# Optimization experiments

Measured on AMD Instinct MI355X. Metric: run time of the kernel, lower is better.

## Reference

```python
import jax, jax.numpy as jnp
import numpy as np

NEG_SLOPE = 0.2
EPS = 1e-16


def gatv2_conv(x, src, dst, n_nodes, Wl, Wr, att, bias):
    """GATv2Conv, heads=1, add_self_loops handled by caller via src/dst.
    x: [N, Fin]; src/dst: [E] (message j->i means src=j, dst=i).
    Wl, Wr: [Fin, Fout]; att: [Fout]; bias: [Fout].
    """
    xl = x @ Wl  # [N, Fout] (source transform)
    xr = x @ Wr  # [N, Fout] (target transform)
    # per-edge attention logit: a^T LeakyReLU(xl[j] + xr[i])
    h = xl[src] + xr[dst]                      # [E, Fout]
    e = jax.nn.leaky_relu(h, NEG_SLOPE) @ att  # [E]
    # segment softmax over incoming edges of each dst node
    m = jax.ops.segment_max(e, dst, num_segments=n_nodes)   # [N]
    ex = jnp.exp(e - m[dst])                                 # [E]
    denom = jax.ops.segment_sum(ex, dst, num_segments=n_nodes)  # [N]
    alpha = ex / (denom[dst] + EPS)                          # [E]
    # scatter-aggregate weighted source messages
    out = jax.ops.segment_sum(alpha[:, None] * xl[src], dst, num_segments=n_nodes)
    return out + bias


def glorot(key, shape):
    lim = np.sqrt(6.0 / (shape[0] + shape[1]))
    return jax.random.uniform(key, shape, jnp.float32, -lim, lim)


def setup_inputs() -> dict:
    key = jax.random.key(0)
    ks = jax.random.split(key, 9)
    N, E, Fin, H, Fout = 50000, 800000, 128, 64, 2
    x = jax.random.normal(ks[0], (N, Fin), jnp.float32)
    edge_index = jax.random.randint(ks[1], (2, E), 0, N, jnp.int64)
    return {
        "x": x,
        "edge_index": edge_index,
        "Wl1": glorot(ks[2], (Fin, H)),
        "Wr1": glorot(ks[3], (Fin, H)),
        "att1": glorot(ks[4], (H, 1))[:, 0],
        "b1": jnp.zeros((H,), jnp.float32),
        "Wl2": glorot(ks[5], (H, Fout)),
        "Wr2": glorot(ks[6], (H, Fout)),
        "att2": glorot(ks[7], (Fout, 1))[:, 0],
        "b2": jnp.zeros((Fout,), jnp.float32),
    }


def reference(x, edge_index, Wl1, Wr1, att1, b1, Wl2, Wr2, att2, b2):
    n_nodes = x.shape[0]
    # PyG GATv2Conv adds self-loops by default
    loops = jnp.arange(n_nodes, dtype=edge_index.dtype)
    src = jnp.concatenate([edge_index[0], loops])
    dst = jnp.concatenate([edge_index[1], loops])
    # eval mode: dropout is identity; the initial relu/dropout result is dead code
    h = gatv2_conv(x, src, dst, n_nodes, Wl1, Wr1, att1, b1)
    out = gatv2_conv(h, src, dst, n_nodes, Wl2, Wr2, att2, b2)
    return out
```

## Files before the change

kernel.cpp:

```cpp
#include <hip/hip_runtime.h>
#include <math.h>

#define FIN 128
#define H 64
#define FOUT 2
#define NEG_SLOPE 0.2f
#define EPS 1e-16f

#define BM 64
#define BK 32
#define SCAN_CHUNK 2048

__global__ void k_zero_int(int* __restrict__ a, int n){
  int i = blockIdx.x*blockDim.x + threadIdx.x;
  if(i < n) a[i] = 0;
}

__global__ __launch_bounds__(256) void k_gemm1(
    const float* __restrict__ x, const float* __restrict__ Wl,
    const float* __restrict__ Wr, float* __restrict__ xl,
    float* __restrict__ xr, int N){
  __shared__ float xsT[BK][BM+4];
  __shared__ float ws[BK][128];
  int tid = threadIdx.x;
  int rowbase = blockIdx.x*BM;
  int tc = tid & 15, tr = tid >> 4;
  int r0 = tr*4, c0 = tc*4;
  float acc[4][8];
  #pragma unroll
  for(int i=0;i<4;i++)
    #pragma unroll
    for(int j=0;j<8;j++) acc[i][j]=0.f;

  int lrow = tid >> 2;
  int lk8  = (tid & 3) * 8;
  int wkk  = tid >> 3;
  int wfq  = tid & 7;

  for(int k0=0; k0<FIN; k0+=BK){
    __syncthreads();
    {
      int grow = rowbase + lrow;
      float4 v0 = make_float4(0,0,0,0), v1 = make_float4(0,0,0,0);
      if(grow < N){
        v0 = *(const float4*)(x + (size_t)grow*FIN + k0 + lk8);
        v1 = *(const float4*)(x + (size_t)grow*FIN + k0 + lk8 + 4);
      }
      xsT[lk8+0][lrow]=v0.x; xsT[lk8+1][lrow]=v0.y; xsT[lk8+2][lrow]=v0.z; xsT[lk8+3][lrow]=v0.w;
      xsT[lk8+4][lrow]=v1.x; xsT[lk8+5][lrow]=v1.y; xsT[lk8+6][lrow]=v1.z; xsT[lk8+7][lrow]=v1.w;
    }
    #pragma unroll
    for(int i=0;i<4;i++){
      int c4 = (wfq + i*8)*4;
      const float* srcp = (c4 < 64) ? (Wl + (size_t)(k0+wkk)*H + c4)
                                    : (Wr + (size_t)(k0+wkk)*H + (c4-64));
      *(float4*)(&ws[wkk][c4]) = *(const float4*)srcp;
    }
    __syncthreads();
    #pragma unroll
    for(int kk=0; kk<BK; kk++){
      float4 av = *(float4*)(&xsT[kk][r0]);
      float4 b0 = *(float4*)(&ws[kk][c0]);
      float4 b1 = *(float4*)(&ws[kk][64+c0]);
      float a[4] = {av.x,av.y,av.z,av.w};
      float b[8] = {b0.x,b0.y,b0.z,b0.w,b1.x,b1.y,b1.z,b1.w};
      #pragma unroll
      for(int i=0;i<4;i++)
        #pragma unroll
        for(int j=0;j<8;j++)
          acc[i][j] += a[i]*b[j];
    }
  }
  #pragma unroll
  for(int i=0;i<4;i++){
    int row = rowbase + r0 + i;
    if(row < N){
      *(float4*)(xl + (size_t)row*H + c0) = make_float4(acc[i][0],acc[i][1],acc[i][2],acc[i][3]);
      *(float4*)(xr + (size_t)row*H + c0) = make_float4(acc[i][4],acc[i][5],acc[i][6],acc[i][7]);
    }
  }
}

__global__ void k_degree(const int* __restrict__ ei, int E, int Etot,
                         int* __restrict__ deg, int* __restrict__ rank){
  int i0 = (blockIdx.x*blockDim.x + threadIdx.x)*4;
  if(i0 >= Etot) return;
  if(i0 + 4 <= E && (E & 3) == 0){
    int4 d4 = *(const int4*)(ei + E + i0);
    int r0 = atomicAdd(&deg[d4.x],1);
    int r1 = atomicAdd(&deg[d4.y],1);
    int r2 = atomicAdd(&deg[d4.z],1);
    int r3 = atomicAdd(&deg[d4.w],1);
    *(int4*)(rank + i0) = make_int4(r0,r1,r2,r3);
  } else if(i0 >= E && i0 + 4 <= Etot){
    int v = i0 - E;
    int r0 = atomicAdd(&deg[v+0],1);
    int r1 = atomicAdd(&deg[v+1],1);
    int r2 = atomicAdd(&deg[v+2],1);
    int r3 = atomicAdd(&deg[v+3],1);
    *(int4*)(rank + i0) = make_int4(r0,r1,r2,r3);
  } else {
    #pragma unroll
    for(int q=0;q<4;q++){
      int i = i0+q; if(i>=Etot) break;
      int dst = (i<E) ? ei[E+i] : (i-E);
      rank[i] = atomicAdd(&deg[dst],1);
    }
  }
}

__global__ __launch_bounds__(256) void k_scan_a(const int* __restrict__ deg, int n,
                                                int* __restrict__ rowptr,
                                                int* __restrict__ blocksum){
  __shared__ int wsum[4];
  int tid = threadIdx.x, lane = tid & 63, wid = tid >> 6;
  int idx = blockIdx.x*SCAN_CHUNK + tid*8;
  int v[8];
  if(idx + 8 <= n){
    int4 a = *(const int4*)(deg + idx);
    int4 b = *(const int4*)(deg + idx + 4);
    v[0]=a.x;v[1]=a.y;v[2]=a.z;v[3]=a.w;v[4]=b.x;v[5]=b.y;v[6]=b.z;v[7]=b.w;
  } else {
    #pragma unroll
    for(int i=0;i<8;i++) v[i] = (idx+i<n)? deg[idx+i] : 0;
  }
  int pre[8]; int st=0;
  #pragma unroll
  for(int i=0;i<8;i++){ pre[i]=st; st+=v[i]; }
  int incl = st;
  #pragma unroll
  for(int o=1;o<64;o<<=1){ int u=__shfl_up(incl,o); if(lane>=o) incl+=u; }
  if(lane==63) wsum[wid]=incl;
  __syncthreads();
  if(tid==0){ int accu=0; for(int i=0;i<4;i++){ int t=wsum[i]; wsum[i]=accu; accu+=t; } }
  __syncthreads();
  int toff = wsum[wid] + incl - st;
  if(idx + 8 <= n){
    int4 o0 = make_int4(toff+pre[0],toff+pre[1],toff+pre[2],toff+pre[3]);
    int4 o1 = make_int4(toff+pre[4],toff+pre[5],toff+pre[6],toff+pre[7]);
    *(int4*)(rowptr+idx)=o0; *(int4*)(rowptr+idx+4)=o1;
  } else {
    #pragma unroll
    for(int i=0;i<8;i++) if(idx+i<n) rowptr[idx+i]=toff+pre[i];
  }
  if(tid==255) blocksum[blockIdx.x] = toff + st;
}

__global__ void k_scan_b(int* __restrict__ blocksum, int nb, int* __restrict__ rowptr, int n){
  int lane = threadIdx.x & 63;
  int v = (lane<nb)? blocksum[lane] : 0;
  int incl = v;
  #pragma unroll
  for(int o=1;o<64;o<<=1){ int u=__shfl_up(incl,o); if(lane>=o) incl+=u; }
  if(lane<nb) blocksum[lane] = incl - v;
  if(lane==63) rowptr[n] = incl;
}

__global__ void k_scan_c(int* __restrict__ rowptr, const int* __restrict__ blocksum, int n){
  int i = blockIdx.x*blockDim.x + threadIdx.x;
  if(i<n) rowptr[i] += blocksum[i >> 11];
}

__global__ void k_fill(const int* __restrict__ ei, int E, int Etot,
                       const int* __restrict__ rowptr,
                       const int* __restrict__ rank, int* __restrict__ csr_src){
  int i0 = (blockIdx.x*blockDim.x + threadIdx.x)*4;
  if(i0 >= Etot) return;
  if(i0 + 4 <= E && (E & 3) == 0){
    int4 s4 = *(const int4*)(ei + i0);
    int4 d4 = *(const int4*)(ei + E + i0);
    int4 r4 = *(const int4*)(rank + i0);
    csr_src[rowptr[d4.x] + r4.x] = s4.x;
    csr_src[rowptr[d4.y] + r4.y] = s4.y;
    csr_src[rowptr[d4.z] + r4.z] = s4.z;
    csr_src[rowptr[d4.w] + r4.w] = s4.w;
  } else if(i0 >= E && i0 + 4 <= Etot){
    int4 r4 = *(const int4*)(rank + i0);
    int v = i0 - E;
    csr_src[rowptr[v+0] + r4.x] = v+0;
    csr_src[rowptr[v+1] + r4.y] = v+1;
    csr_src[rowptr[v+2] + r4.z] = v+2;
    csr_src[rowptr[v+3] + r4.w] = v+3;
  } else {
    #pragma unroll
    for(int q=0;q<4;q++){
      int i = i0+q; if(i>=Etot) break;
      int src, dst;
      if(i<E){ src = ei[i]; dst = ei[E+i]; } else { src = i-E; dst = i-E; }
      csr_src[rowptr[dst] + rank[i]] = src;
    }
  }
}

__global__ void k_node1f(const int* __restrict__ rowptr, const int* __restrict__ csr_src,
                         const float* __restrict__ xl, const float* __restrict__ xr,
                         const float* __restrict__ att, const float* __restrict__ b1,
                         const float* __restrict__ Wl2, const float* __restrict__ Wr2,
                         float* __restrict__ xl2, float* __restrict__ xr2, int N){
  int node = blockIdx.x*16 + (threadIdx.x>>4);
  int gl = threadIdx.x & 15;
  if(node >= N) return;
  int f4 = gl*4;
  float4 attv = *(const float4*)(att + f4);
  float4 xrv  = *(const float4*)(xr + (size_t)node*H + f4);
  int s = rowptr[node], t = rowptr[node+1];
  float d = 0.f;
  float ax=0.f, ay=0.f, az=0.f, aw=0.f;

  for(int k=s; k<t; k+=8){
    int tl = t - 1;
    int ks[8]; float4 xv[8]; float msk[8];
    #pragma unroll
    for(int j=0;j<8;j++){
      int kj = k + j;
      ks[j] = (kj < t) ? kj : tl;
      msk[j] = (kj < t) ? 1.f : 0.f;
    }
    int ss[8];
    #pragma unroll
    for(int j=0;j<8;j++) ss[j] = csr_src[ks[j]];
    #pragma unroll
    for(int j=0;j<8;j++) xv[j] = *(const float4*)(xl + (size_t)ss[j]*H + f4);
    #pragma unroll
    for(int j=0;j<8;j++){
      float h0 = xv[j].x + xrv.x, h1 = xv[j].y + xrv.y;
      float h2 = xv[j].z + xrv.z, h3 = xv[j].w + xrv.w;
      float l0 = (h0>0.f)? h0 : NEG_SLOPE*h0;
      float l1 = (h1>0.f)? h1 : NEG_SLOPE*h1;
      float l2 = (h2>0.f)? h2 : NEG_SLOPE*h2;
      float l3 = (h3>0.f)? h3 : NEG_SLOPE*h3;
      float e = l0*attv.x + l1*attv.y + l2*attv.z + l3*attv.w;
      #pragma unroll
      for(int o=1;o<16;o<<=1) e += __shfl_xor(e,o);
      float w = msk[j] * __expf(e);
      d  += w;
      ax += w*xv[j].x; ay += w*xv[j].y; az += w*xv[j].z; aw += w*xv[j].w;
    }
  }

  float inv = 1.f/(d + EPS);
  float4 bv = *(const float4*)(b1 + f4);
  float h0 = ax*inv + bv.x, h1 = ay*inv + bv.y;
  float h2 = az*inv + bv.z, h3 = aw*inv + bv.w;
  float p0 = h0*Wl2[(f4+0)*FOUT+0] + h1*Wl2[(f4+1)*FOUT+0] + h2*Wl2[(f4+2)*FOUT+0] + h3*Wl2[(f4+3)*FOUT+0];
  float p1 = h0*Wl2[(f4+0)*FOUT+1] + h1*Wl2[(f4+1)*FOUT+1] + h2*Wl2[(f4+2)*FOUT+1] + h3*Wl2[(f4+3)*FOUT+1];
  float p2 = h0*Wr2[(f4+0)*FOUT+0] + h1*Wr2[(f4+1)*FOUT+0] + h2*Wr2[(f4+2)*FOUT+0] + h3*Wr2[(f4+3)*FOUT+0];
  float p3 = h0*Wr2[(f4+0)*FOUT+1] + h1*Wr2[(f4+1)*FOUT+1] + h2*Wr2[(f4+2)*FOUT+1] + h3*Wr2[(f4+3)*FOUT+1];
  #pragma unroll
  for(int o=1;o<16;o<<=1){
    p0 += __shfl_xor(p0,o); p1 += __shfl_xor(p1,o);
    p2 += __shfl_xor(p2,o); p3 += __shfl_xor(p3,o);
  }
  if(gl==0){
    *(float2*)(xl2 + node*2) = make_float2(p0,p1);
    *(float2*)(xr2 + node*2) = make_float2(p2,p3);
  }
}

__global__ void k_node2(const int* __restrict__ rowptr, const int* __restrict__ csr_src,
                        const float* __restrict__ xl2, const float* __restrict__ xr2,
                        const float* __restrict__ att2, const float* __restrict__ b2,
                        float* __restrict__ out, int N){
  int node = blockIdx.x*16 + (threadIdx.x>>4);
  int gl = threadIdx.x & 15;
  if(node >= N) return;
  int s = rowptr[node], t = rowptr[node+1];
  float2 xrv = *(const float2*)(xr2 + node*2);
  float a0 = att2[0], a1 = att2[1];
  float den=0.f, n0=0.f, n1=0.f;
  for(int k=s+gl; k<t; k+=16){
    int src = csr_src[k];
    float2 xs = *(const float2*)(xl2 + src*2);
    float h0 = xs.x + xrv.x, h1 = xs.y + xrv.y;
    float l0 = (h0>0.f)? h0 : NEG_SLOPE*h0;
    float l1 = (h1>0.f)? h1 : NEG_SLOPE*h1;
    float ex = __expf(l0*a0 + l1*a1);
    den += ex; n0 += ex*xs.x; n1 += ex*xs.y;
  }
  #pragma unroll
  for(int o=1;o<16;o<<=1){
    den += __shfl_xor(den,o);
    n0  += __shfl_xor(n0,o);
    n1  += __shfl_xor(n1,o);
  }
  if(gl==0){
    float inv = 1.f/(den + EPS);
    out[node*2+0] = n0*inv + b2[0];
    out[node*2+1] = n1*inv + b2[1];
  }
}

extern "C" void kernel_launch(void* const* d_in, const int* in_sizes, int n_in,
                              void* d_out, int out_size, void* d_ws, size_t ws_size,
                              hipStream_t stream){
  const float* x    = (const float*)d_in[0];
  const int*   ei   = (const int*)d_in[1];
  const float* Wl1  = (const float*)d_in[2];
  const float* Wr1  = (const float*)d_in[3];
  const float* att1 = (const float*)d_in[4];
  const float* b1   = (const float*)d_in[5];
  const float* Wl2  = (const float*)d_in[6];
  const float* Wr2  = (const float*)d_in[7];
  const float* att2 = (const float*)d_in[8];
  const float* b2   = (const float*)d_in[9];
  int N = in_sizes[0]/FIN;
  int E = in_sizes[1]/2;
  int Etot = E + N;
  int nscan = (N + SCAN_CHUNK - 1) / SCAN_CHUNK;
  int nquad = (Etot + 3) / 4;

  char* w = (char*)d_ws;
  size_t off = 0;
  auto alloc = [&](size_t bytes)->void*{
    void* p = w + off;
    off = (off + bytes + 255) & ~(size_t)255;
    return p;
  };
  float* xl1     = (float*)alloc((size_t)N*H*4);
  float* xr1     = (float*)alloc((size_t)N*H*4);
  int*   csr_src = (int*)  alloc((size_t)Etot*4);
  int*   rank    = (int*)  alloc((size_t)Etot*4);
  int*   deg     = (int*)  alloc((size_t)N*4);
  int*   rowptr  = (int*)  alloc((size_t)(N+1)*4);
  int*   blocksum= (int*)  alloc((size_t)64*4);
  float* xl2     = (float*)alloc((size_t)N*2*4);
  float* xr2     = (float*)alloc((size_t)N*2*4);

  k_zero_int<<<(N+511)/512,512,0,stream>>>(deg, N);
  k_gemm1<<<(N+BM-1)/BM, 256, 0, stream>>>(x, Wl1, Wr1, xl1, xr1, N);
  k_degree<<<(nquad+255)/256,256,0,stream>>>(ei, E, Etot, deg, rank);
  k_scan_a<<<nscan,256,0,stream>>>(deg, N, rowptr, blocksum);
  k_scan_b<<<1,64,0,stream>>>(blocksum, nscan, rowptr, N);
  k_scan_c<<<(N+255)/256,256,0,stream>>>(rowptr, blocksum, N);
  k_fill<<<(nquad+255)/256,256,0,stream>>>(ei, E, Etot, rowptr, rank, csr_src);
  k_node1f<<<(N+15)/16, 256, 0, stream>>>(rowptr, csr_src, xl1, xr1, att1, b1, Wl2, Wr2, xl2, xr2, N);
  k_node2<<<(N+15)/16, 256, 0, stream>>>(rowptr, csr_src, xl2, xr2, att2, b2, (float*)d_out, N);
}
```

Before: 135.2 us.

## Fuse degree counting into GEMM launch and fold scan fix-up into consumers

The degree/rank atomic kernel and the first-layer GEMM now run in one launch, with the first GD blocks doing the atomics and the rest doing GEMM tiles, so the two independent jobs overlap. The single-block scan_b and the elementwise scan_c kernels are removed. Instead, fill, node1f and node2 each scan the per-chunk block sums into shared memory and add the chunk offset when they read rowptr. This cuts three launches and one pass over rowptr, at the cost of a small redundant scan in every consumer block. It also relies on rowptr[N] being handled correctly through the last chunk's offset.

Measured after the change: 130.5 us. 3.5% less time.

```diff
diff --git a/kernel.cpp b/kernel.cpp
--- a/kernel.cpp
+++ b/kernel.cpp
@@ -16,14 +16,57 @@
   if(i < n) a[i] = 0;
 }
 
-__global__ __launch_bounds__(256) void k_gemm1(
+__device__ __forceinline__ void load_bs(const int* __restrict__ blocksum, int nscan,
+                                        int* bs, int tid){
+  if(tid < 64){
+    int v = (tid < nscan)? blocksum[tid] : 0;
+    int incl = v;
+    #pragma unroll
+    for(int o=1;o<64;o<<=1){ int u=__shfl_up(incl,o); if(tid>=o) incl+=u; }
+    bs[tid] = incl - v;
+  }
+  __syncthreads();
+}
+
+__global__ __launch_bounds__(256) void k_deg_gemm(
+    const int* __restrict__ ei, int E, int Etot,
+    int* __restrict__ deg, int* __restrict__ rank, int GD,
     const float* __restrict__ x, const float* __restrict__ Wl,
     const float* __restrict__ Wr, float* __restrict__ xl,
     float* __restrict__ xr, int N){
   __shared__ float xsT[BK][BM+4];
   __shared__ float ws[BK][128];
   int tid = threadIdx.x;
-  int rowbase = blockIdx.x*BM;
+
+  if((int)blockIdx.x < GD){
+    int i0 = (blockIdx.x*256 + tid)*4;
+    if(i0 >= Etot) return;
+    if(i0 + 4 <= E && (E & 3) == 0){
+      int4 d4 = *(const int4*)(ei + E + i0);
+      int r0 = atomicAdd(&deg[d4.x],1);
+      int r1 = atomicAdd(&deg[d4.y],1);
+      int r2 = atomicAdd(&deg[d4.z],1);
+      int r3 = atomicAdd(&deg[d4.w],1);
+      *(int4*)(rank + i0) = make_int4(r0,r1,r2,r3);
+    } else if(i0 >= E && i0 + 4 <= Etot){
+      int v = i0 - E;
+      int r0 = atomicAdd(&deg[v+0],1);
+      int r1 = atomicAdd(&deg[v+1],1);
+      int r2 = atomicAdd(&deg[v+2],1);
+      int r3 = atomicAdd(&deg[v+3],1);
+      *(int4*)(rank + i0) = make_int4(r0,r1,r2,r3);
+    } else {
+      #pragma unroll
+      for(int q=0;q<4;q++){
+        int i = i0+q; if(i>=Etot) break;
+        int dst = (i<E) ? ei[E+i] : (i-E);
+        rank[i] = atomicAdd(&deg[dst],1);
+      }
+    }
+    return;
+  }
+
+  int rowbase = (blockIdx.x - GD)*BM;
   int tc = tid & 15, tr = tid >> 4;
   int r0 = tr*4, c0 = tc*4;
   float acc[4][8];
@@ -77,34 +120,6 @@
     if(row < N){
       *(float4*)(xl + (size_t)row*H + c0) = make_float4(acc[i][0],acc[i][1],acc[i][2],acc[i][3]);
       *(float4*)(xr + (size_t)row*H + c0) = make_float4(acc[i][4],acc[i][5],acc[i][6],acc[i][7]);
-    }
-  }
-}
-
-__global__ void k_degree(const int* __restrict__ ei, int E, int Etot,
-                         int* __restrict__ deg, int* __restrict__ rank){
-  int i0 = (blockIdx.x*blockDim.x + threadIdx.x)*4;
-  if(i0 >= Etot) return;
-  if(i0 + 4 <= E && (E & 3) == 0){
-    int4 d4 = *(const int4*)(ei + E + i0);
-    int r0 = atomicAdd(&deg[d4.x],1);
-    int r1 = atomicAdd(&deg[d4.y],1);
-    int r2 = atomicAdd(&deg[d4.z],1);
-    int r3 = atomicAdd(&deg[d4.w],1);
-    *(int4*)(rank + i0) = make_int4(r0,r1,r2,r3);
-  } else if(i0 >= E && i0 + 4 <= Etot){
-    int v = i0 - E;
-    int r0 = atomicAdd(&deg[v+0],1);
-    int r1 = atomicAdd(&deg[v+1],1);
-    int r2 = atomicAdd(&deg[v+2],1);
-    int r3 = atomicAdd(&deg[v+3],1);
-    *(int4*)(rank + i0) = make_int4(r0,r1,r2,r3);
-  } else {
-    #pragma unroll
-    for(int q=0;q<4;q++){
-      int i = i0+q; if(i>=Etot) break;
-      int dst = (i<E) ? ei[E+i] : (i-E);
-      rank[i] = atomicAdd(&deg[dst],1);
     }
   }
 }
@@ -143,67 +158,64 @@
     #pragma unroll
     for(int i=0;i<8;i++) if(idx+i<n) rowptr[idx+i]=toff+pre[i];
   }
-  if(tid==255) blocksum[blockIdx.x] = toff + st;
-}
-
-__global__ void k_scan_b(int* __restrict__ blocksum, int nb, int* __restrict__ rowptr, int n){
-  int lane = threadIdx.x & 63;
-  int v = (lane<nb)? blocksum[lane] : 0;
-  int incl = v;
-  #pragma unroll
-  for(int o=1;o<64;o<<=1){ int u=__shfl_up(incl,o); if(lane>=o) incl+=u; }
-  if(lane<nb) blocksum[lane] = incl - v;
-  if(lane==63) rowptr[n] = incl;
-}
-
-__global__ void k_scan_c(int* __restrict__ rowptr, const int* __restrict__ blocksum, int n){
-  int i = blockIdx.x*blockDim.x + threadIdx.x;
-  if(i<n) rowptr[i] += blocksum[i >> 11];
+  if(tid==255){
+    blocksum[blockIdx.x] = toff + st;
+    if(blockIdx.x == gridDim.x-1) rowptr[n] = toff + st;
+  }
 }
 
 __global__ void k_fill(const int* __restrict__ ei, int E, int Etot,
                        const int* __restrict__ rowptr,
+                       const int* __restrict__ blocksum, int nscan,
                        const int* __restrict__ rank, int* __restrict__ csr_src){
-  int i0 = (blockIdx.x*blockDim.x + threadIdx.x)*4;
+  __shared__ int bs[64];
+  int tid = threadIdx.x;
+  load_bs(blocksum, nscan, bs, tid);
+  int i0 = (blockIdx.x*blockDim.x + tid)*4;
   if(i0 >= Etot) return;
   if(i0 + 4 <= E && (E & 3) == 0){
     int4 s4 = *(const int4*)(ei + i0);
     int4 d4 = *(const int4*)(ei + E + i0);
     int4 r4 = *(const int4*)(rank + i0);
-    csr_src[rowptr[d4.x] + r4.x] = s4.x;
-    csr_src[rowptr[d4.y] + r4.y] = s4.y;
-    csr_src[rowptr[d4.z] + r4.z] = s4.z;
-    csr_src[rowptr[d4.w] + r4.w] = s4.w;
+    csr_src[rowptr[d4.x] + bs[d4.x>>11] + r4.x] = s4.x;
+    csr_src[rowptr[d4.y] + bs[d4.y>>11] + r4.y] = s4.y;
+    csr_src[rowptr[d4.z] + bs[d4.z>>11] + r4.z] = s4.z;
+    csr_src[rowptr[d4.w] + bs[d4.w>>11] + r4.w] = s4.w;
   } else if(i0 >= E && i0 + 4 <= Etot){
     int4 r4 = *(const int4*)(rank + i0);
     int v = i0 - E;
-    csr_src[rowptr[v+0] + r4.x] = v+0;
-    csr_src[rowptr[v+1] + r4.y] = v+1;
-    csr_src[rowptr[v+2] + r4.z] = v+2;
-    csr_src[rowptr[v+3] + r4.w] = v+3;
+    csr_src[rowptr[v+0] + bs[(v+0)>>11] + r4.x] = v+0;
+    csr_src[rowptr[v+1] + bs[(v+1)>>11] + r4.y] = v+1;
+    csr_src[rowptr[v+2] + bs[(v+2)>>11] + r4.z] = v+2;
+    csr_src[rowptr[v+3] + bs[(v+3)>>11] + r4.w] = v+3;
   } else {
     #pragma unroll
     for(int q=0;q<4;q++){
       int i = i0+q; if(i>=Etot) break;
       int src, dst;
       if(i<E){ src = ei[i]; dst = ei[E+i]; } else { src = i-E; dst = i-E; }
-      csr_src[rowptr[dst] + rank[i]] = src;
-    }
-  }
-}
-
-__global__ void k_node1f(const int* __restrict__ rowptr, const int* __restrict__ csr_src,
+      csr_src[rowptr[dst] + bs[dst>>11] + rank[i]] = src;
+    }
+  }
+}
+
+__global__ void k_node1f(const int* __restrict__ rowptr, const int* __restrict__ blocksum,
+                         int nscan, const int* __restrict__ csr_src,
                          const float* __restrict__ xl, const float* __restrict__ xr,
                          const float* __restrict__ att, const float* __restrict__ b1,
                          const float* __restrict__ Wl2, const float* __restrict__ Wr2,
                          float* __restrict__ xl2, float* __restrict__ xr2, int N){
-  int node = blockIdx.x*16 + (threadIdx.x>>4);
-  int gl = threadIdx.x & 15;
+  __shared__ int bs[64];
+  int tid = threadIdx.x;
+  load_bs(blocksum, nscan, bs, tid);
+  int node = blockIdx.x*16 + (tid>>4);
+  int gl = tid & 15;
   if(node >= N) return;
   int f4 = gl*4;
   float4 attv = *(const float4*)(att + f4);
   float4 xrv  = *(const float4*)(xr + (size_t)node*H + f4);
-  int s = rowptr[node], t = rowptr[node+1];
+  int s = rowptr[node]   + bs[node>>11];
+  int t = rowptr[node+1] + bs[(node+1)>>11];
   float d = 0.f;
   float ax=0.f, ay=0.f, az=0.f, aw=0.f;
 
@@ -257,14 +269,19 @@
   }
 }
 
-__global__ void k_node2(const int* __restrict__ rowptr, const int* __restrict__ csr_src,
+__global__ void k_node2(const int* __restrict__ rowptr, const int* __restrict__ blocksum,
+                        int nscan, const int* __restrict__ csr_src,
                         const float* __restrict__ xl2, const float* __restrict__ xr2,
                         const float* __restrict__ att2, const float* __restrict__ b2,
                         float* __restrict__ out, int N){
-  int node = blockIdx.x*16 + (threadIdx.x>>4);
-  int gl = threadIdx.x & 15;
+  __shared__ int bs[64];
+  int tid = threadIdx.x;
+  load_bs(blocksum, nscan, bs, tid);
+  int node = blockIdx.x*16 + (tid>>4);
+  int gl = tid & 15;
   if(node >= N) return;
-  int s = rowptr[node], t = rowptr[node+1];
+  int s = rowptr[node]   + bs[node>>11];
+  int t = rowptr[node+1] + bs[(node+1)>>11];
   float2 xrv = *(const float2*)(xr2 + node*2);
   float a0 = att2[0], a1 = att2[1];
   float den=0.f, n0=0.f, n1=0.f;
@@ -308,6 +325,8 @@
   int Etot = E + N;
   int nscan = (N + SCAN_CHUNK - 1) / SCAN_CHUNK;
   int nquad = (Etot + 3) / 4;
+  int GD = (nquad + 255) / 256;
+  int GG = (N + BM - 1) / BM;
 
   char* w = (char*)d_ws;
   size_t off = 0;
@@ -327,12 +346,12 @@
   float* xr2     = (float*)alloc((size_t)N*2*4);
 
   k_zero_int<<<(N+511)/512,512,0,stream>>>(deg, N);
-  k_gemm1<<<(N+BM-1)/BM, 256, 0, stream>>>(x, Wl1, Wr1, xl1, xr1, N);
-  k_degree<<<(nquad+255)/256,256,0,stream>>>(ei, E, Etot, deg, rank);
+  k_deg_gemm<<<GD+GG, 256, 0, stream>>>(ei, E, Etot, deg, rank, GD,
+                                        x, Wl1, Wr1, xl1, xr1, N);
   k_scan_a<<<nscan,256,0,stream>>>(deg, N, rowptr, blocksum);
-  k_scan_b<<<1,64,0,stream>>>(blocksum, nscan, rowptr, N);
-  k_scan_c<<<(N+255)/256,256,0,stream>>>(rowptr, blocksum, N);
-  k_fill<<<(nquad+255)/256,256,0,stream>>>(ei, E, Etot, rowptr, rank, csr_src);
-  k_node1f<<<(N+15)/16, 256, 0, stream>>>(rowptr, csr_src, xl1, xr1, att1, b1, Wl2, Wr2, xl2, xr2, N);
-  k_node2<<<(N+15)/16, 256, 0, stream>>>(rowptr, csr_src, xl2, xr2, att2, b2, (float*)d_out, N);
-}
+  k_fill<<<GD,256,0,stream>>>(ei, E, Etot, rowptr, blocksum, nscan, rank, csr_src);
+  k_node1f<<<(N+15)/16, 256, 0, stream>>>(rowptr, blocksum, nscan, csr_src,
+                                          xl1, xr1, att1, b1, Wl2, Wr2, xl2, xr2, N);
+  k_node2<<<(N+15)/16, 256, 0, stream>>>(rowptr, blocksum, nscan, csr_src,
+                                         xl2, xr2, att2, b2, (float*)d_out, N);
+}
```
